# Performance work log

Hardware: AMD Instinct MI355X
Metric: run time of the kernel (lower is better)

## Reference

```python
import jax, jax.numpy as jnp
import numpy as np

HEADS = 16
DIM_HEAD = 64
QUERY_DIM = 1024
INNER = HEADS * DIM_HEAD
SCALE = DIM_HEAD ** -0.5


def setup_inputs() -> dict:
    key = jax.random.key(0)
    ks = jax.random.split(key, 6)
    B, N, M = 2, 2048, 2048
    x = jax.random.normal(ks[0], (B, N, QUERY_DIM), dtype=jnp.float32)
    context = jax.random.normal(ks[1], (B, M, QUERY_DIM), dtype=jnp.float32)
    s = QUERY_DIM ** -0.5
    # weights stored [in, out] so y = x @ W matches torch Linear(x) with W = weight.T
    Wq = jax.random.normal(ks[2], (QUERY_DIM, INNER), dtype=jnp.float32) * s
    Wk = jax.random.normal(ks[3], (QUERY_DIM, INNER), dtype=jnp.float32) * s
    Wv = jax.random.normal(ks[4], (QUERY_DIM, INNER), dtype=jnp.float32) * s
    Wo = jax.random.normal(ks[5], (INNER, QUERY_DIM), dtype=jnp.float32) * (INNER ** -0.5)
    return {"x": x, "context": context, "Wq": Wq, "Wk": Wk, "Wv": Wv, "Wo": Wo}


def reference(x, context, Wq, Wk, Wv, Wo):
    B, N, _ = x.shape
    M = context.shape[1]
    # projections -> [b, n, h, d]
    q = (x @ Wq).reshape(B, N, HEADS, DIM_HEAD)
    k = (context @ Wk).reshape(B, M, HEADS, DIM_HEAD)
    v = (context @ Wv).reshape(B, M, HEADS, DIM_HEAD)
    sim = jnp.einsum('bihd,bjhd->bhij', q, k) * SCALE  # [b, h, n, m]
    attn = jax.nn.softmax(sim, axis=-1)
    out = jnp.einsum('bhij,bjhd->bihd', attn, v)  # [b, n, h, d]
    out = out.reshape(B, N, INNER)
    return out @ Wo
```

## Files before the change

### kernel.cpp

```cpp
#include <hip/hip_runtime.h>
#include <hip/hip_bf16.h>


typedef __attribute__((ext_vector_type(8))) __bf16    bf16x8;
typedef __attribute__((ext_vector_type(4))) __bf16    bf16x4;
typedef __attribute__((ext_vector_type(4))) float     f32x4;

#define B_    2
#define H_    16
#define N_    2048
#define M_    2048
#define D_    64
#define QD_   1024

#define QSCALE 0.18033688011112042f

__device__ __forceinline__ void gld16(const __bf16* g, __bf16* l) {
    __builtin_amdgcn_global_load_lds(
        (const __attribute__((address_space(1))) unsigned int*)(g),
        (__attribute__((address_space(3))) unsigned int*)(l), 16, 0, 0);
}

__global__ __launch_bounds__(256) void prep(const float* __restrict__ x,
                                            const float* __restrict__ ctx,
                                            const float* __restrict__ w0,
                                            const float* __restrict__ w1,
                                            const float* __restrict__ w2,
                                            const float* __restrict__ w3,
                                            __bf16* __restrict__ xb,
                                            __bf16* __restrict__ cb,
                                            __bf16* __restrict__ t0,
                                            __bf16* __restrict__ t1,
                                            __bf16* __restrict__ t2,
                                            __bf16* __restrict__ t3) {
    __shared__ float tile[64][65];
    const int z = blockIdx.z;
    if (z < 2) {
        const float* src = z ? ctx : x;
        __bf16*      dst = z ? cb  : xb;
        const size_t base = (size_t)(blockIdx.y * 16 + blockIdx.x) * 16384;
#pragma unroll
        for (int p = 0; p < 16; ++p) {
            size_t i = base + p * 1024 + threadIdx.x * 4;
            float4 v = *reinterpret_cast<const float4*>(src + i);
            bf16x4 o;
            o.x = (__bf16)v.x; o.y = (__bf16)v.y; o.z = (__bf16)v.z; o.w = (__bf16)v.w;
            *reinterpret_cast<bf16x4*>(dst + i) = o;
        }
        return;
    }
    const int w = z - 2;
    const float* in = (w == 0) ? w0 : (w == 1) ? w1 : (w == 2) ? w2 : w3;
    __bf16*     out = (w == 0) ? t0 : (w == 1) ? t1 : (w == 2) ? t2 : t3;
    const int i0 = blockIdx.x * 64;
    const int o0 = blockIdx.y * 64;
    const int t  = threadIdx.x;
    const int r  = t >> 4;
    const int c4 = (t & 15) * 4;
#pragma unroll
    for (int p = 0; p < 4; ++p) {
        int row = p * 16 + r;
        float4 v = *reinterpret_cast<const float4*>(in + (size_t)(i0 + row) * QD_ + o0 + c4);
        tile[row][c4 + 0] = v.x; tile[row][c4 + 1] = v.y;
        tile[row][c4 + 2] = v.z; tile[row][c4 + 3] = v.w;
    }
    __syncthreads();
#pragma unroll
    for (int p = 0; p < 4; ++p) {
        int orow = p * 16 + r;
        bf16x4 o;
        o.x = (__bf16)tile[c4 + 0][orow];
        o.y = (__bf16)tile[c4 + 1][orow];
        o.z = (__bf16)tile[c4 + 2][orow];
        o.w = (__bf16)tile[c4 + 3][orow];
        *reinterpret_cast<bf16x4*>(out + (size_t)(o0 + orow) * QD_ + i0 + c4) = o;
    }
}

__global__ __launch_bounds__(256) void gemm_qkv(const __bf16* __restrict__ xb,
                                                const __bf16* __restrict__ cb,
                                                const __bf16* __restrict__ Wtq,
                                                const __bf16* __restrict__ Wtk,
                                                const __bf16* __restrict__ Wtv,
                                                __bf16* __restrict__ Qb,
                                                __bf16* __restrict__ Kb,
                                                __bf16* __restrict__ Vt) {
    __shared__ __align__(16) __bf16 POOL[16384];
    __bf16* const Al0 = POOL;
    __bf16* const Al1 = POOL + 4096;
    __bf16* const Bl0 = POOL + 8192;
    __bf16* const Bl1 = POOL + 12288;

    const int z = blockIdx.z;
    const __bf16* A_  = (z == 0) ? xb : cb;
    const __bf16* Bt_ = (z == 0) ? Wtq : (z == 1) ? Wtk : Wtv;

    const int tid  = threadIdx.x;
    const int wid  = tid >> 6;
    const int lane = tid & 63;
    const int l15  = lane & 15;
    const int lg   = lane >> 4;
    const int wr   = wid >> 1;
    const int wc   = wid & 1;
    const int rowBase = blockIdx.x * 128;
    const int colBase = blockIdx.y * 128;
    const int srow = wid * 32 + (lane >> 2);
    const int sg   = ((lane & 3) ^ ((srow >> 1) & 3)) * 8;
    const __bf16* Ag  = A_  + (size_t)(rowBase + srow) * QD_ + sg;
    const __bf16* Ag2 = Ag  + (size_t)16 * QD_;
    const __bf16* Bg  = Bt_ + (size_t)(colBase + srow) * QD_ + sg;
    const __bf16* Bg2 = Bg  + (size_t)16 * QD_;
    const int sOff  = (wid * 32) * 32;
    const int sOff2 = sOff + 16 * 32;
    int aoff[4], boff[4];
#pragma unroll
    for (int m = 0; m < 4; ++m) {
        int ra = wr * 64 + m * 16 + l15;
        int rb = wc * 64 + m * 16 + l15;
        aoff[m] = ra * 32 + ((lg ^ ((ra >> 1) & 3)) * 8);
        boff[m] = rb * 32 + ((lg ^ ((rb >> 1) & 3)) * 8);
    }
    f32x4 acc[4][4] = {};

#define GCOMPUTE(AL, BL)                                                                       \
    {                                                                                          \
        bf16x8 a[4], b[4];                                                                     \
        _Pragma("unroll")                                                                      \
        for (int m = 0; m < 4; ++m)                                                            \
            a[m] = *reinterpret_cast<const bf16x8*>(&(AL)[aoff[m]]);                           \
        _Pragma("unroll")                                                                      \
        for (int n = 0; n < 4; ++n)                                                            \
            b[n] = *reinterpret_cast<const bf16x8*>(&(BL)[boff[n]]);                           \
        _Pragma("unroll")                                                                      \
        for (int m = 0; m < 4; ++m)                                                            \
            _Pragma("unroll")                                                                  \
            for (int n = 0; n < 4; ++n)                                                        \
                acc[m][n] = __builtin_amdgcn_mfma_f32_16x16x32_bf16(a[m], b[n], acc[m][n], 0, 0, 0); \
    }

    gld16(Ag,  Al0 + sOff);
    gld16(Ag2, Al0 + sOff2);
    gld16(Bg,  Bl0 + sOff);
    gld16(Bg2, Bl0 + sOff2);
    __syncthreads();
    for (int t = 0; t < 32; t += 2) {
        if (t + 1 < 32) {
            int kn = (t + 1) * 32;
            gld16(Ag + kn,  Al1 + sOff);
            gld16(Ag2 + kn, Al1 + sOff2);
            gld16(Bg + kn,  Bl1 + sOff);
            gld16(Bg2 + kn, Bl1 + sOff2);
        }
        GCOMPUTE(Al0, Bl0)
        __syncthreads();
        if (t + 2 < 32) {
            int kn = (t + 2) * 32;
            gld16(Ag + kn,  Al0 + sOff);
            gld16(Ag2 + kn, Al0 + sOff2);
            gld16(Bg + kn,  Bl0 + sOff);
            gld16(Bg2 + kn, Bl0 + sOff2);
        }
        GCOMPUTE(Al1, Bl1)
        __syncthreads();
    }
#undef GCOMPUTE

#pragma unroll
    for (int m = 0; m < 4; ++m)
#pragma unroll
        for (int n = 0; n < 4; ++n)
#pragma unroll
            for (int r = 0; r < 4; ++r) {
                float v = acc[m][n][r];
                if (z == 0) v *= QSCALE;
                int rl = wr * 64 + m * 16 + lg * 4 + r;
                int cl = wc * 64 + n * 16 + l15;
                if (z == 2) POOL[cl * 128 + rl] = (__bf16)v;
                else        POOL[rl * 128 + cl] = (__bf16)v;
            }
    __syncthreads();

    const int prow0 = tid >> 4;
    const int pcol  = (tid & 15) * 8;
#pragma unroll
    for (int s = 0; s < 8; ++s) {
        int row = s * 16 + prow0;
        bf16x8 vv = *reinterpret_cast<const bf16x8*>(&POOL[row * 128 + pcol]);
        if (z == 2) {
            int cc = colBase + row, rr = rowBase + pcol;
            int b_ = rr >> 11, mm = rr & 2047, hh = cc >> 6, dd = cc & 63;
            *reinterpret_cast<bf16x8*>(&Vt[((size_t)(b_ * H_ + hh) * D_ + dd) * M_ + mm]) = vv;
        } else {
            int rr = rowBase + row, cc = colBase + pcol;
            int b_ = rr >> 11, nn = rr & 2047, hh = cc >> 6, dd = cc & 63;
            __bf16* dst = (z == 0) ? Qb : Kb;
            *reinterpret_cast<bf16x8*>(&dst[((size_t)(b_ * H_ + hh) * N_ + nn) * D_ + dd]) = vv;
        }
    }
}

__global__ __launch_bounds__(256) void gemm_out(const __bf16* __restrict__ AO,
                                                const __bf16* __restrict__ Wto,
                                                float* __restrict__ out) {
    __shared__ __align__(16) __bf16 POOL[16384];
    __bf16* const Al0 = POOL;
    __bf16* const Al1 = POOL + 4096;
    __bf16* const Bl0 = POOL + 8192;
    __bf16* const Bl1 = POOL + 10240;

    const int tid  = threadIdx.x;
    const int wid  = tid >> 6;
    const int lane = tid & 63;
    const int l15  = lane & 15;
    const int lg   = lane >> 4;
    const int wr   = wid >> 1;
    const int wc   = wid & 1;
    const int rowBase = blockIdx.x * 128;
    const int colBase = blockIdx.y * 64;
    const int srowA = wid * 32 + (lane >> 2);
    const int srowB = wid * 16 + (lane >> 2);
    const int sgA   = ((lane & 3) ^ ((srowA >> 1) & 3)) * 8;
    const int sgB   = ((lane & 3) ^ ((srowB >> 1) & 3)) * 8;
    const __bf16* Ag  = AO  + (size_t)(rowBase + srowA) * QD_ + sgA;
    const __bf16* Ag2 = Ag  + (size_t)16 * QD_;
    const __bf16* Bg  = Wto + (size_t)(colBase + srowB) * QD_ + sgB;
    const int sOffA  = (wid * 32) * 32;
    const int sOffA2 = sOffA + 16 * 32;
    const int sOffB  = (wid * 16) * 32;
    int aoff[4], boff[2];
#pragma unroll
    for (int m = 0; m < 4; ++m) {
        int ra = wr * 64 + m * 16 + l15;
        aoff[m] = ra * 32 + ((lg ^ ((ra >> 1) & 3)) * 8);
    }
#pragma unroll
    for (int n = 0; n < 2; ++n) {
        int rb = wc * 32 + n * 16 + l15;
        boff[n] = rb * 32 + ((lg ^ ((rb >> 1) & 3)) * 8);
    }
    f32x4 acc[4][2] = {};

#define GCOMPUTE2(AL, BL)                                                                      \
    {                                                                                          \
        bf16x8 a[4], b[2];                                                                     \
        _Pragma("unroll")                                                                      \
        for (int m = 0; m < 4; ++m)                                                            \
            a[m] = *reinterpret_cast<const bf16x8*>(&(AL)[aoff[m]]);                           \
        _Pragma("unroll")                                                                      \
        for (int n = 0; n < 2; ++n)                                                            \
            b[n] = *reinterpret_cast<const bf16x8*>(&(BL)[boff[n]]);                           \
        _Pragma("unroll")                                                                      \
        for (int m = 0; m < 4; ++m)                                                            \
            _Pragma("unroll")                                                                  \
            for (int n = 0; n < 2; ++n)                                                        \
                acc[m][n] = __builtin_amdgcn_mfma_f32_16x16x32_bf16(a[m], b[n], acc[m][n], 0, 0, 0); \
    }

    gld16(Ag,  Al0 + sOffA);
    gld16(Ag2, Al0 + sOffA2);
    gld16(Bg,  Bl0 + sOffB);
    __syncthreads();
    for (int t = 0; t < 32; t += 2) {
        if (t + 1 < 32) {
            int kn = (t + 1) * 32;
            gld16(Ag + kn,  Al1 + sOffA);
            gld16(Ag2 + kn, Al1 + sOffA2);
            gld16(Bg + kn,  Bl1 + sOffB);
        }
        GCOMPUTE2(Al0, Bl0)
        __syncthreads();
        if (t + 2 < 32) {
            int kn = (t + 2) * 32;
            gld16(Ag + kn,  Al0 + sOffA);
            gld16(Ag2 + kn, Al0 + sOffA2);
            gld16(Bg + kn,  Bl0 + sOffB);
        }
        GCOMPUTE2(Al1, Bl1)
        __syncthreads();
    }
#undef GCOMPUTE2

    float* FP = reinterpret_cast<float*>(POOL);
#pragma unroll
    for (int m = 0; m < 4; ++m)
#pragma unroll
        for (int n = 0; n < 2; ++n)
#pragma unroll
            for (int r = 0; r < 4; ++r) {
                int rl = wr * 64 + m * 16 + lg * 4 + r;
                int cl = wc * 32 + n * 16 + l15;
                FP[rl * 64 + cl] = acc[m][n][r];
            }
    __syncthreads();
    const int prow0 = tid >> 4;
    const int pcol4 = (tid & 15) * 4;
#pragma unroll
    for (int s = 0; s < 8; ++s) {
        int row = s * 16 + prow0;
        float4 vv = *reinterpret_cast<const float4*>(&FP[row * 64 + pcol4]);
        *reinterpret_cast<float4*>(&out[(size_t)(rowBase + row) * QD_ + colBase + pcol4]) = vv;
    }
}

__global__ __launch_bounds__(256) void attn_kernel(const __bf16* __restrict__ Q,
                                                   const __bf16* __restrict__ K,
                                                   const __bf16* __restrict__ Vt,
                                                   __bf16* __restrict__ AO) {
    __shared__ __align__(16) __bf16 Klds[2][4096];
    __shared__ __align__(16) __bf16 Vlds[2][4096];

    const int logical = (blockIdx.x & 7) * 64 + (blockIdx.x >> 3);
    const int qt   = logical & 15;
    const int bh   = logical >> 4;
    const int b    = bh >> 4;
    const int h    = bh & 15;
    const int wid  = threadIdx.x >> 6;
    const int lane = threadIdx.x & 63;
    const int l15  = lane & 15;
    const int lg   = lane >> 4;
    const int qbase = qt * 128 + wid * 32;

    const __bf16* Qp = Q  + ((size_t)bh * N_ + qbase) * D_;
    const __bf16* Kp = K  + (size_t)bh * M_ * D_;
    const __bf16* Vp = Vt + (size_t)bh * D_ * M_;

    const int srow = (wid << 4) + (lane >> 3);
    const int scol = (lane & 7) << 3;
    const int sk0  = (lane >> 3) & 3;
    const int sk1  = sk0 | 4;
    const int sv   = lane >> 3;
    const int kc0  = scol ^ (sk0 << 3);
    const int kc1  = scol ^ (sk1 << 3);
    const int vc   = scol ^ (sv  << 3);
    __bf16* kl0 = &Klds[0][wid * 1024];
    __bf16* kl1 = &Klds[1][wid * 1024];
    __bf16* vl0 = &Vlds[0][wid * 1024];
    __bf16* vl1 = &Vlds[1][wid * 1024];

#define STAGE(KL, VL, KV0)                                                     \
    gld16(Kp + (size_t)((KV0) + srow)     * D_ + kc0, (KL));                   \
    gld16(Kp + (size_t)((KV0) + srow + 8) * D_ + kc1, (KL) + 512);             \
    gld16(Vp + (size_t)(srow)     * M_ + (KV0) + vc,  (VL));                   \
    gld16(Vp + (size_t)(srow + 8) * M_ + (KV0) + vc,  (VL) + 512);

    const int rm0 = ((l15 >> 2) * 8) + (l15 & 3);
    const int skq = (l15 & 3) | (((l15 >> 2) & 1) << 2);
    const int svq = l15 & 7;
    const int ak00 = rm0 * 64 + (( 0 + lg * 8) ^ (skq << 3));
    const int ak01 = rm0 * 64 + ((32 + lg * 8) ^ (skq << 3));
    const int ak10 = ak00 + 256;
    const int ak11 = ak01 + 256;
    const int av0 = l15 * 64 + (( 0 + lg * 8) ^ (svq << 3));
    const int av1 = l15 * 64 + ((32 + lg * 8) ^ (svq << 3));

    bf16x8 qf00 = *reinterpret_cast<const bf16x8*>(Qp + (size_t)(l15)      * D_ +      lg * 8);
    bf16x8 qf01 = *reinterpret_cast<const bf16x8*>(Qp + (size_t)(l15)      * D_ + 32 + lg * 8);
    bf16x8 qf10 = *reinterpret_cast<const bf16x8*>(Qp + (size_t)(16 + l15) * D_ +      lg * 8);
    bf16x8 qf11 = *reinterpret_cast<const bf16x8*>(Qp + (size_t)(16 + l15) * D_ + 32 + lg * 8);

    bf16x8 onesf;
#pragma unroll
    for (int j = 0; j < 8; ++j) onesf[j] = (__bf16)1.0f;

    f32x4 o00 = {}, o01 = {}, o10 = {}, o11 = {};
    f32x4 o20 = {}, o21 = {}, o30 = {}, o31 = {};
    f32x4 ors0 = {}, ors1 = {};

#define COMPUTE(KB, VB, KOFF, AV)                                                               \
    {                                                                                           \
        bf16x8 k00 = *reinterpret_cast<const bf16x8*>((KB) + ak00 + (KOFF));                    \
        bf16x8 k01 = *reinterpret_cast<const bf16x8*>((KB) + ak01 + (KOFF));                    \
        bf16x8 k10 = *reinterpret_cast<const bf16x8*>((KB) + ak10 + (KOFF));                    \
        bf16x8 k11 = *reinterpret_cast<const bf16x8*>((KB) + ak11 + (KOFF));                    \
        bf16x8 v0  = *reinterpret_cast<const bf16x8*>((VB) + (AV));                             \
        bf16x8 v1  = *reinterpret_cast<const bf16x8*>((VB) + (AV) + 1024);                      \
        bf16x8 v2  = *reinterpret_cast<const bf16x8*>((VB) + (AV) + 2048);                      \
        bf16x8 v3  = *reinterpret_cast<const bf16x8*>((VB) + (AV) + 3072);                      \
        f32x4 s00 = {}, s01 = {}, s10 = {}, s11 = {};                                           \
        s00 = __builtin_amdgcn_mfma_f32_16x16x32_bf16(k00, qf00, s00, 0, 0, 0);                 \
        s00 = __builtin_amdgcn_mfma_f32_16x16x32_bf16(k01, qf01, s00, 0, 0, 0);                 \
        s01 = __builtin_amdgcn_mfma_f32_16x16x32_bf16(k00, qf10, s01, 0, 0, 0);                 \
        s01 = __builtin_amdgcn_mfma_f32_16x16x32_bf16(k01, qf11, s01, 0, 0, 0);                 \
        s10 = __builtin_amdgcn_mfma_f32_16x16x32_bf16(k10, qf00, s10, 0, 0, 0);                 \
        s10 = __builtin_amdgcn_mfma_f32_16x16x32_bf16(k11, qf01, s10, 0, 0, 0);                 \
        s11 = __builtin_amdgcn_mfma_f32_16x16x32_bf16(k10, qf10, s11, 0, 0, 0);                 \
        s11 = __builtin_amdgcn_mfma_f32_16x16x32_bf16(k11, qf11, s11, 0, 0, 0);                 \
        bf16x8 pf0, pf1;                                                                        \
        pf0[0] = (__bf16)__builtin_amdgcn_exp2f(s00[0]);                                        \
        pf0[1] = (__bf16)__builtin_amdgcn_exp2f(s00[1]);                                        \
        pf0[2] = (__bf16)__builtin_amdgcn_exp2f(s00[2]);                                        \
        pf0[3] = (__bf16)__builtin_amdgcn_exp2f(s00[3]);                                        \
        pf0[4] = (__bf16)__builtin_amdgcn_exp2f(s10[0]);                                        \
        pf0[5] = (__bf16)__builtin_amdgcn_exp2f(s10[1]);                                        \
        pf0[6] = (__bf16)__builtin_amdgcn_exp2f(s10[2]);                                        \
        pf0[7] = (__bf16)__builtin_amdgcn_exp2f(s10[3]);                                        \
        pf1[0] = (__bf16)__builtin_amdgcn_exp2f(s01[0]);                                        \
        pf1[1] = (__bf16)__builtin_amdgcn_exp2f(s01[1]);                                        \
        pf1[2] = (__bf16)__builtin_amdgcn_exp2f(s01[2]);                                        \
        pf1[3] = (__bf16)__builtin_amdgcn_exp2f(s01[3]);                                        \
        pf1[4] = (__bf16)__builtin_amdgcn_exp2f(s11[0]);                                        \
        pf1[5] = (__bf16)__builtin_amdgcn_exp2f(s11[1]);                                        \
        pf1[6] = (__bf16)__builtin_amdgcn_exp2f(s11[2]);                                        \
        pf1[7] = (__bf16)__builtin_amdgcn_exp2f(s11[3]);                                        \
        ors0 = __builtin_amdgcn_mfma_f32_16x16x32_bf16(pf0, onesf, ors0, 0, 0, 0);              \
        ors1 = __builtin_amdgcn_mfma_f32_16x16x32_bf16(pf1, onesf, ors1, 0, 0, 0);              \
        o00 = __builtin_amdgcn_mfma_f32_16x16x32_bf16(pf0, v0, o00, 0, 0, 0);                   \
        o01 = __builtin_amdgcn_mfma_f32_16x16x32_bf16(pf1, v0, o01, 0, 0, 0);                   \
        o10 = __builtin_amdgcn_mfma_f32_16x16x32_bf16(pf0, v1, o10, 0, 0, 0);                   \
        o11 = __builtin_amdgcn_mfma_f32_16x16x32_bf16(pf1, v1, o11, 0, 0, 0);                   \
        o20 = __builtin_amdgcn_mfma_f32_16x16x32_bf16(pf0, v2, o20, 0, 0, 0);                   \
        o21 = __builtin_amdgcn_mfma_f32_16x16x32_bf16(pf1, v2, o21, 0, 0, 0);                   \
        o30 = __builtin_amdgcn_mfma_f32_16x16x32_bf16(pf0, v3, o30, 0, 0, 0);                   \
        o31 = __builtin_amdgcn_mfma_f32_16x16x32_bf16(pf1, v3, o31, 0, 0, 0);                   \
    }

    STAGE(kl0, vl0, 0)
    __syncthreads();

    for (int t = 0; t < 32; t += 2) {
        if (t + 1 < 32) { STAGE(kl1, vl1, (t + 1) * 64) }
        COMPUTE(Klds[0], Vlds[0], 0,    av0)
        COMPUTE(Klds[0], Vlds[0], 2048, av1)
        __syncthreads();
        if (t + 2 < 32) { STAGE(kl0, vl0, (t + 2) * 64) }
        COMPUTE(Klds[1], Vlds[1], 0,    av0)
        COMPUTE(Klds[1], Vlds[1], 2048, av1)
        __syncthreads();
    }
#undef STAGE
#undef COMPUTE

#pragma unroll
    for (int r = 0; r < 4; ++r) {
        float i0 = 1.0f / ors0[r];
        float i1 = 1.0f / ors1[r];
        size_t row0 = ((size_t)b * N_ + qbase + lg * 4 + r) * QD_ + h * D_ + l15;
        size_t row1 = ((size_t)b * N_ + qbase + 16 + lg * 4 + r) * QD_ + h * D_ + l15;
        AO[row0 +  0] = (__bf16)(o00[r] * i0);
        AO[row0 + 16] = (__bf16)(o10[r] * i0);
        AO[row0 + 32] = (__bf16)(o20[r] * i0);
        AO[row0 + 48] = (__bf16)(o30[r] * i0);
        AO[row1 +  0] = (__bf16)(o01[r] * i1);
        AO[row1 + 16] = (__bf16)(o11[r] * i1);
        AO[row1 + 32] = (__bf16)(o21[r] * i1);
        AO[row1 + 48] = (__bf16)(o31[r] * i1);
    }
}

extern "C" void kernel_launch(void* const* d_in, const int* in_sizes, int n_in,
                              void* d_out, int out_size, void* d_ws, size_t ws_size,
                              hipStream_t stream) {
    const float* x   = (const float*)d_in[0];
    const float* ctx = (const float*)d_in[1];
    const float* Wq  = (const float*)d_in[2];
    const float* Wk  = (const float*)d_in[3];
    const float* Wv  = (const float*)d_in[4];
    const float* Wo  = (const float*)d_in[5];

    char* ws = (char*)d_ws;
    __bf16* xb  = (__bf16*)(ws);
    __bf16* cb  = (__bf16*)(ws + (8u  << 20));
    __bf16* Wtq = (__bf16*)(ws + (16u << 20));
    __bf16* Wtk = (__bf16*)(ws + (18u << 20));
    __bf16* Wtv = (__bf16*)(ws + (20u << 20));
    __bf16* Wto = (__bf16*)(ws + (22u << 20));
    __bf16* Qb  = (__bf16*)(ws + (24u << 20));
    __bf16* Kb  = (__bf16*)(ws + (32u << 20));
    __bf16* Vt  = (__bf16*)(ws + (40u << 20));
    __bf16* AO  = (__bf16*)(ws + (48u << 20));

    prep<<<dim3(16, 16, 6), 256, 0, stream>>>(x, ctx, Wq, Wk, Wv, Wo,
                                              xb, cb, Wtq, Wtk, Wtv, Wto);
    gemm_qkv<<<dim3(32, 8, 3), 256, 0, stream>>>(xb, cb, Wtq, Wtk, Wtv, Qb, Kb, Vt);
    attn_kernel<<<512, 256, 0, stream>>>(Qb, Kb, Vt, AO);
    gemm_out<<<dim3(32, 16), 256, 0, stream>>>(AO, Wto, (float*)d_out);
}
```

Before: 113.8 us.

## Split attention KV range across two wave groups and merge partial results in LDS

Doubles the attention block to 512 threads. Two groups of four waves each process half of the 2048 keys for the same 128 queries, then combine their partial outputs and row sums through shared memory before normalising. This is meant to give each CU more waves to hide latency and to halve the serial KV loop per wave. The cost is more LDS per block, an extra LDS reduction with a barrier at the end, and different occupancy under launch_bounds(512,4). The unnormalised exp (no running max) lets the partial sums be added directly.

```diff
diff --git a/kernel.cpp b/kernel.cpp
--- a/kernel.cpp
+++ b/kernel.cpp
@@ -302,12 +302,11 @@
     }
 }
 
-__global__ __launch_bounds__(256) void attn_kernel(const __bf16* __restrict__ Q,
-                                                   const __bf16* __restrict__ K,
-                                                   const __bf16* __restrict__ Vt,
-                                                   __bf16* __restrict__ AO) {
-    __shared__ __align__(16) __bf16 Klds[2][4096];
-    __shared__ __align__(16) __bf16 Vlds[2][4096];
+__global__ __launch_bounds__(512, 4) void attn_kernel(const __bf16* __restrict__ Q,
+                                                      const __bf16* __restrict__ K,
+                                                      const __bf16* __restrict__ Vt,
+                                                      __bf16* __restrict__ AO) {
+    __shared__ __align__(16) __bf16 POOL[32768];
 
     const int logical = (blockIdx.x & 7) * 64 + (blockIdx.x >> 3);
     const int qt   = logical & 15;
@@ -315,16 +314,19 @@
     const int b    = bh >> 4;
     const int h    = bh & 15;
     const int wid  = threadIdx.x >> 6;
+    const int grp  = wid >> 2;
+    const int wl   = wid & 3;
     const int lane = threadIdx.x & 63;
     const int l15  = lane & 15;
     const int lg   = lane >> 4;
-    const int qbase = qt * 128 + wid * 32;
+    const int qbase = qt * 128 + wl * 32;
+    const int kv0   = grp << 10;
 
     const __bf16* Qp = Q  + ((size_t)bh * N_ + qbase) * D_;
     const __bf16* Kp = K  + (size_t)bh * M_ * D_;
     const __bf16* Vp = Vt + (size_t)bh * D_ * M_;
 
-    const int srow = (wid << 4) + (lane >> 3);
+    const int srow = (wl << 4) + (lane >> 3);
     const int scol = (lane & 7) << 3;
     const int sk0  = (lane >> 3) & 3;
     const int sk1  = sk0 | 4;
@@ -332,16 +334,21 @@
     const int kc0  = scol ^ (sk0 << 3);
     const int kc1  = scol ^ (sk1 << 3);
     const int vc   = scol ^ (sv  << 3);
-    __bf16* kl0 = &Klds[0][wid * 1024];
-    __bf16* kl1 = &Klds[1][wid * 1024];
-    __bf16* vl0 = &Vlds[0][wid * 1024];
-    __bf16* vl1 = &Vlds[1][wid * 1024];
-
-#define STAGE(KL, VL, KV0)                                                     \
-    gld16(Kp + (size_t)((KV0) + srow)     * D_ + kc0, (KL));                   \
-    gld16(Kp + (size_t)((KV0) + srow + 8) * D_ + kc1, (KL) + 512);             \
-    gld16(Vp + (size_t)(srow)     * M_ + (KV0) + vc,  (VL));                   \
-    gld16(Vp + (size_t)(srow + 8) * M_ + (KV0) + vc,  (VL) + 512);
+
+    __bf16* const K0 = POOL + (grp * 2 + 0) * 4096;
+    __bf16* const K1 = POOL + (grp * 2 + 1) * 4096;
+    __bf16* const V0 = POOL + 16384 + (grp * 2 + 0) * 4096;
+    __bf16* const V1 = POOL + 16384 + (grp * 2 + 1) * 4096;
+    __bf16* const k0d = K0 + wl * 1024;
+    __bf16* const k1d = K1 + wl * 1024;
+    __bf16* const v0d = V0 + wl * 1024;
+    __bf16* const v1d = V1 + wl * 1024;
+
+#define STAGE(KD, VD, KV)                                                      \
+    gld16(Kp + (size_t)((KV) + srow)     * D_ + kc0, (KD));                    \
+    gld16(Kp + (size_t)((KV) + srow + 8) * D_ + kc1, (KD) + 512);              \
+    gld16(Vp + (size_t)(srow)     * M_ + (KV) + vc,  (VD));                    \
+    gld16(Vp + (size_t)(srow + 8) * M_ + (KV) + vc,  (VD) + 512);
 
     const int rm0 = ((l15 >> 2) * 8) + (l15 & 3);
     const int skq = (l15 & 3) | (((l15 >> 2) & 1) << 2);
@@ -414,36 +421,59 @@
         o31 = __builtin_amdgcn_mfma_f32_16x16x32_bf16(pf1, v3, o31, 0, 0, 0);                   \
     }
 
-    STAGE(kl0, vl0, 0)
-    __syncthreads();
-
-    for (int t = 0; t < 32; t += 2) {
-        if (t + 1 < 32) { STAGE(kl1, vl1, (t + 1) * 64) }
-        COMPUTE(Klds[0], Vlds[0], 0,    av0)
-        COMPUTE(Klds[0], Vlds[0], 2048, av1)
+    STAGE(k0d, v0d, kv0)
+    __syncthreads();
+
+    for (int t = 0; t < 16; t += 2) {
+        if (t + 1 < 16) { STAGE(k1d, v1d, kv0 + (t + 1) * 64) }
+        COMPUTE(K0, V0, 0,    av0)
+        COMPUTE(K0, V0, 2048, av1)
         __syncthreads();
-        if (t + 2 < 32) { STAGE(kl0, vl0, (t + 2) * 64) }
-        COMPUTE(Klds[1], Vlds[1], 0,    av0)
-        COMPUTE(Klds[1], Vlds[1], 2048, av1)
+        if (t + 2 < 16) { STAGE(k0d, v0d, kv0 + (t + 2) * 64) }
+        COMPUTE(K1, V1, 0,    av0)
+        COMPUTE(K1, V1, 2048, av1)
         __syncthreads();
     }
 #undef STAGE
 #undef COMPUTE
 
-#pragma unroll
-    for (int r = 0; r < 4; ++r) {
-        float i0 = 1.0f / ors0[r];
-        float i1 = 1.0f / ors1[r];
-        size_t row0 = ((size_t)b * N_ + qbase + lg * 4 + r) * QD_ + h * D_ + l15;
-        size_t row1 = ((size_t)b * N_ + qbase + 16 + lg * 4 + r) * QD_ + h * D_ + l15;
-        AO[row0 +  0] = (__bf16)(o00[r] * i0);
-        AO[row0 + 16] = (__bf16)(o10[r] * i0);
-        AO[row0 + 32] = (__bf16)(o20[r] * i0);
-        AO[row0 + 48] = (__bf16)(o30[r] * i0);
-        AO[row1 +  0] = (__bf16)(o01[r] * i1);
-        AO[row1 + 16] = (__bf16)(o11[r] * i1);
-        AO[row1 + 32] = (__bf16)(o21[r] * i1);
-        AO[row1 + 48] = (__bf16)(o31[r] * i1);
+    float* LO = reinterpret_cast<float*>(POOL);
+    float* LS = LO + 128 * 65;
+    if (grp == 1) {
+#pragma unroll
+        for (int r = 0; r < 4; ++r) {
+            int row0 = wl * 32 + lg * 4 + r;
+            int row1 = row0 + 16;
+            LO[row0 * 65 +  0 + l15] = o00[r];
+            LO[row0 * 65 + 16 + l15] = o10[r];
+            LO[row0 * 65 + 32 + l15] = o20[r];
+            LO[row0 * 65 + 48 + l15] = o30[r];
+            LO[row1 * 65 +  0 + l15] = o01[r];
+            LO[row1 * 65 + 16 + l15] = o11[r];
+            LO[row1 * 65 + 32 + l15] = o21[r];
+            LO[row1 * 65 + 48 + l15] = o31[r];
+            if (l15 == 0) { LS[row0] = ors0[r]; LS[row1] = ors1[r]; }
+        }
+    }
+    __syncthreads();
+    if (grp == 0) {
+#pragma unroll
+        for (int r = 0; r < 4; ++r) {
+            int row0 = wl * 32 + lg * 4 + r;
+            int row1 = row0 + 16;
+            float i0 = 1.0f / (ors0[r] + LS[row0]);
+            float i1 = 1.0f / (ors1[r] + LS[row1]);
+            size_t g0 = ((size_t)b * N_ + qbase + lg * 4 + r) * QD_ + h * D_ + l15;
+            size_t g1 = ((size_t)b * N_ + qbase + 16 + lg * 4 + r) * QD_ + h * D_ + l15;
+            AO[g0 +  0] = (__bf16)((o00[r] + LO[row0 * 65 +  0 + l15]) * i0);
+            AO[g0 + 16] = (__bf16)((o10[r] + LO[row0 * 65 + 16 + l15]) * i0);
+            AO[g0 + 32] = (__bf16)((o20[r] + LO[row0 * 65 + 32 + l15]) * i0);
+            AO[g0 + 48] = (__bf16)((o30[r] + LO[row0 * 65 + 48 + l15]) * i0);
+            AO[g1 +  0] = (__bf16)((o01[r] + LO[row1 * 65 +  0 + l15]) * i1);
+            AO[g1 + 16] = (__bf16)((o11[r] + LO[row1 * 65 + 16 + l15]) * i1);
+            AO[g1 + 32] = (__bf16)((o21[r] + LO[row1 * 65 + 32 + l15]) * i1);
+            AO[g1 + 48] = (__bf16)((o31[r] + LO[row1 * 65 + 48 + l15]) * i1);
+        }
     }
 }
 
@@ -472,6 +502,6 @@
     prep<<<dim3(16, 16, 6), 256, 0, stream>>>(x, ctx, Wq, Wk, Wv, Wo,
                                               xb, cb, Wtq, Wtk, Wtv, Wto);
     gemm_qkv<<<dim3(32, 8, 3), 256, 0, stream>>>(xb, cb, Wtq, Wtk, Wtv, Qb, Kb, Vt);
-    attn_kernel<<<512, 256, 0, stream>>>(Qb, Kb, Vt, AO);
+    attn_kernel<<<512, 512, 0, stream>>>(Qb, Kb, Vt, AO);
     gemm_out<<<dim3(32, 16), 256, 0, stream>>>(AO, Wto, (float*)d_out);
 }
```

Measured after the change: 105.9 us. -6.9%, faster.
